# Kernel tuning notes

Hardware: AMD Instinct MI355X
Metric: run time of the kernel (lower is better)

Reference implementation:

```python
import jax, jax.numpy as jnp
import numpy as np

H, D = 8, 16  # heads, head_dim (hidden=128)
NEG_SLOPE = 0.2


def _seg_softmax(logits, seg, n):
    # softmax over edges grouped by destination node (leading axis)
    m = jax.ops.segment_max(logits, seg, num_segments=n)
    m = jnp.where(jnp.isfinite(m), m, 0.0)
    e = jnp.exp(logits - m[seg])
    s = jax.ops.segment_sum(e, seg, num_segments=n)
    return e / (s[seg] + 1e-16)


def _edge_type_out(x_src, x_dst, att_s, att_d, src, dst, n_dst):
    # GAT-style node-level attention for one edge type.
    # x_src: [Ns,H,D], x_dst: [Nd,H,D]
    a_s = (x_src * att_s).sum(-1)            # [Ns,H]
    a_d = (x_dst * att_d).sum(-1)            # [Nd,H]
    alpha = a_s[src] + a_d[dst]              # [E,H]
    alpha = jnp.where(alpha >= 0, alpha, NEG_SLOPE * alpha)  # leaky_relu(0.2)
    alpha = _seg_softmax(alpha, dst, n_dst)  # [E,H]
    msg = x_src[src] * alpha[:, :, None]     # [E,H,D]
    out = jax.ops.segment_sum(msg, dst, num_segments=n_dst)  # [Nd,H,D]
    return jax.nn.relu(out.reshape(n_dst, H * D))


def setup_inputs() -> dict:
    key = jax.random.key(0)
    ks = jax.random.split(key, 24)
    Na, Np, Nd = 300000, 150000, 80000
    E = 1000000
    hid = H * D
    inp = {
        "x_adm": jax.random.normal(ks[0], (Na, 128), jnp.float32),
        "x_pat": jax.random.normal(ks[1], (Np, 64), jnp.float32),
        "x_diag": jax.random.normal(ks[2], (Nd, 64), jnp.float32),
        "e_pa_src": jax.random.randint(ks[3], (E,), 0, Np),
        "e_pa_dst": jax.random.randint(ks[4], (E,), 0, Na),
        "e_da_src": jax.random.randint(ks[5], (E,), 0, Nd),
        "e_da_dst": jax.random.randint(ks[6], (E,), 0, Na),
        # per-node-type projections (PyG HANConv proj[node_type])
        "Wa": jax.random.normal(ks[7], (128, hid), jnp.float32) * 0.05,
        "ba": jnp.zeros((hid,), jnp.float32),
        "Wp": jax.random.normal(ks[8], (64, hid), jnp.float32) * 0.05,
        "bp": jnp.zeros((hid,), jnp.float32),
        "Wd": jax.random.normal(ks[9], (64, hid), jnp.float32) * 0.05,
        "bd": jnp.zeros((hid,), jnp.float32),
        # per-edge-type attention vectors [H,D]
        "ats_pa": jax.random.normal(ks[10], (H, D), jnp.float32) * 0.1,
        "atd_pa": jax.random.normal(ks[11], (H, D), jnp.float32) * 0.1,
        "ats_da": jax.random.normal(ks[12], (H, D), jnp.float32) * 0.1,
        "atd_da": jax.random.normal(ks[13], (H, D), jnp.float32) * 0.1,
        # semantic attention
        "Wk": jax.random.normal(ks[14], (hid, hid), jnp.float32) * 0.05,
        "bk": jnp.zeros((hid,), jnp.float32),
        "q": jax.random.normal(ks[15], (hid,), jnp.float32) * 0.1,
        # final classifier Linear(128, 2)
        "Wl": jax.random.normal(ks[16], (hid, 2), jnp.float32) * 0.05,
        "bl": jnp.zeros((2,), jnp.float32),
    }
    return inp


def reference(x_adm, x_pat, x_diag, e_pa_src, e_pa_dst, e_da_src, e_da_dst,
              Wa, ba, Wp, bp, Wd, bd,
              ats_pa, atd_pa, ats_da, atd_da,
              Wk, bk, q, Wl, bl):
    Na = x_adm.shape[0]
    h_a = (x_adm @ Wa + ba).reshape(Na, H, D)
    h_p = (x_pat @ Wp + bp).reshape(-1, H, D)
    h_d = (x_diag @ Wd + bd).reshape(-1, H, D)
    # node-level attention per metapath (dropout=0.6 skipped: eval mode)
    o_pa = _edge_type_out(h_p, h_a, ats_pa, atd_pa, e_pa_src, e_pa_dst, Na)
    o_da = _edge_type_out(h_d, h_a, ats_da, atd_da, e_da_src, e_da_dst, Na)
    # semantic-level attention across metapaths
    stack = jnp.stack([o_pa, o_da])                 # [2,Na,128]
    w = jnp.tanh(stack @ Wk + bk).mean(axis=1)      # [2,128]
    beta = jax.nn.softmax((w * q).sum(-1), axis=0)  # [2]
    sem = (beta[:, None, None] * stack).sum(0)      # [Na,128]
    logits = sem @ Wl + bl
    return jax.nn.softmax(logits, axis=1)
```

## Files before the change

### kernel.cpp

```cpp
#include <hip/hip_runtime.h>
#include <hip/hip_bf16.h>

typedef __hip_bfloat16 bf16;
typedef __attribute__((ext_vector_type(8))) short frag_ab;
typedef __attribute__((ext_vector_type(4))) float frag_cd;

__device__ __forceinline__ short f2bs(float f){
    bf16 h = __float2bfloat16(f); short s; __builtin_memcpy(&s, &h, 2); return s;
}
__device__ __forceinline__ unsigned pack2(float a, float b){
    return (unsigned)(unsigned short)f2bs(a) | (((unsigned)(unsigned short)f2bs(b)) << 16);
}
__device__ __forceinline__ float blo(unsigned u){ return __uint_as_float(u << 16); }
__device__ __forceinline__ float bhi(unsigned u){ return __uint_as_float(u & 0xffff0000u); }
__device__ __forceinline__ float fast_tanh(float x){
    x = fminf(fmaxf(x, -15.f), 15.f);
    const float t = __expf(2.f*x);
    return (t - 1.f) * __builtin_amdgcn_rcpf(t + 1.f);
}
static inline int imin(int a, int b){ return a < b ? a : b; }

__global__ void prep_fold(const float* __restrict__ Wa, const float* __restrict__ ba,
                          const float* __restrict__ atd_pa, const float* __restrict__ atd_da,
                          float* __restrict__ Wf, float* __restrict__ bdot)
{
    const int k = threadIdx.x;
    for (int g = 0; g < 16; g++){
        const float* att = (g < 8) ? atd_pa : atd_da;
        const int h = g & 7;
        float ssum = 0.f;
        for (int d = 0; d < 16; d++)
            ssum += Wa[k*128 + h*16 + d] * att[h*16 + d];
        Wf[k*16 + g] = ssum;
    }
    if (k < 16){
        const float* att = (k < 8) ? atd_pa : atd_da;
        const int h = k & 7;
        float sb = 0.f;
        for (int d = 0; d < 16; d++) sb += ba[h*16 + d] * att[h*16 + d];
        bdot[k] = sb;
    }
}

__global__ __launch_bounds__(256) void afold_kernel(
    const float* __restrict__ x,
    const float* __restrict__ Wf,
    const float* __restrict__ bdot,
    float* __restrict__ a_pa,
    float* __restrict__ a_da,
    int Na, int ntiles)
{
    __shared__ float WfT[16*132];
    __shared__ float xsr[16*132];
    __shared__ float bs[16];
    const int tid = threadIdx.x;
    for (int i = tid; i < 2048; i += 256){
        const int k = i >> 4, g = i & 15;
        WfT[g*132 + k] = Wf[k*16 + g];
    }
    if (tid < 16) bs[tid] = bdot[tid];
    const int r = tid >> 4, g = tid & 15;

    for (int tile = blockIdx.x; tile < ntiles; tile += gridDim.x){
        const int row0 = tile*16;
        __syncthreads();
        for (int i = tid; i < 512; i += 256){
            const int rr = i >> 5, c4 = (i & 31)*4;
            const int row = row0 + rr;
            float4 v = make_float4(0.f,0.f,0.f,0.f);
            if (row < Na) v = *(const float4*)&x[(size_t)row*128 + c4];
            *(float4*)&xsr[rr*132 + c4] = v;
        }
        __syncthreads();
        float acc = bs[g];
        #pragma unroll 4
        for (int k0 = 0; k0 < 128; k0 += 4){
            const float4 xv = *(const float4*)&xsr[r*132 + k0];
            const float4 wv = *(const float4*)&WfT[g*132 + k0];
            acc += xv.x*wv.x + xv.y*wv.y + xv.z*wv.z + xv.w*wv.w;
        }
        const int row = row0 + r;
        if (row < Na){
            if (g < 8) a_pa[(size_t)row*8 + g]     = acc;
            else       a_da[(size_t)row*8 + (g-8)] = acc;
        }
    }
}

__global__ __launch_bounds__(256) void proj64(
    const float* __restrict__ x,
    const float* __restrict__ W,
    const float* __restrict__ b,
    const float* __restrict__ att0,
    bf16*  __restrict__ h_out,
    float* __restrict__ a0_out,
    int N, int ntiles)
{
    constexpr int K = 64;
    __shared__ float Wsf[K*128];
    __shared__ float xs[32*K];
    const int tid = threadIdx.x;
    const int cg = tid & 31;
    const int rg = tid >> 5;

    for (int i = tid; i < K*32; i += 256)
        *(float4*)&Wsf[i*4] = *(const float4*)&W[i*4];

    float bc[4], at0v[4];
    #pragma unroll
    for (int u = 0; u < 4; u++){ bc[u] = b[cg*4+u]; at0v[u] = att0[cg*4+u]; }
    const int head = cg >> 2;

    for (int tile = blockIdx.x; tile < ntiles; tile += gridDim.x){
        const int row0 = tile*32;
        __syncthreads();
        for (int i = tid; i < 32*(K/4); i += 256){
            const int r  = i / (K/4);
            const int c4 = (i % (K/4))*4;
            const int row = row0 + r;
            float4 v = make_float4(0.f,0.f,0.f,0.f);
            if (row < N) v = *(const float4*)&x[(size_t)row*K + c4];
            *(float4*)&xs[r*K + c4] = v;
        }
        __syncthreads();

        float acc[4][4];
        #pragma unroll
        for (int j = 0; j < 4; j++){ acc[j][0]=acc[j][1]=acc[j][2]=acc[j][3]=0.f; }

        #pragma unroll 2
        for (int k0 = 0; k0 < K; k0 += 4){
            float xr[4][4];
            #pragma unroll
            for (int j = 0; j < 4; j++){
                const float4 v = *(const float4*)&xs[(rg*4+j)*K + k0];
                xr[j][0]=v.x; xr[j][1]=v.y; xr[j][2]=v.z; xr[j][3]=v.w;
            }
            #pragma unroll
            for (int kk = 0; kk < 4; kk++){
                const float4 wv = *(const float4*)&Wsf[(k0+kk)*128 + cg*4];
                #pragma unroll
                for (int j = 0; j < 4; j++){
                    acc[j][0] = fmaf(xr[j][kk], wv.x, acc[j][0]);
                    acc[j][1] = fmaf(xr[j][kk], wv.y, acc[j][1]);
                    acc[j][2] = fmaf(xr[j][kk], wv.z, acc[j][2]);
                    acc[j][3] = fmaf(xr[j][kk], wv.w, acc[j][3]);
                }
            }
        }

        #pragma unroll
        for (int j = 0; j < 4; j++){
            const int row = row0 + rg*4 + j;
            const bool valid = row < N;
            const float h0 = acc[j][0]+bc[0], h1 = acc[j][1]+bc[1];
            const float h2 = acc[j][2]+bc[2], h3 = acc[j][3]+bc[3];
            if (valid){
                h_out[(size_t)row*128 + cg*4+0] = __float2bfloat16(h0);
                h_out[(size_t)row*128 + cg*4+1] = __float2bfloat16(h1);
                h_out[(size_t)row*128 + cg*4+2] = __float2bfloat16(h2);
                h_out[(size_t)row*128 + cg*4+3] = __float2bfloat16(h3);
            }
            float p0 = h0*at0v[0] + h1*at0v[1] + h2*at0v[2] + h3*at0v[3];
            p0 += __shfl_down(p0, 2, 4);
            p0 += __shfl_down(p0, 1, 4);
            if (valid && (cg & 3) == 0) a0_out[(size_t)row*8 + head] = p0;
        }
    }
}

__global__ __launch_bounds__(256) void hist_kernel(
    const int* __restrict__ dst, int* __restrict__ cnt, int E)
{
    const int e = blockIdx.x*256 + threadIdx.x;
    if (e < E) atomicAdd(&cnt[dst[e]], 1);
}

__global__ __launch_bounds__(256) void scan_bsum(
    const int* __restrict__ cnt, int* __restrict__ bsum, int n)
{
    __shared__ int red[256];
    const int base = blockIdx.x*4096;
    int s = 0;
    for (int i = threadIdx.x; i < 4096; i += 256){
        const int idx = base + i;
        s += (idx < n) ? cnt[idx] : 0;
    }
    red[threadIdx.x] = s; __syncthreads();
    for (int st = 128; st > 0; st >>= 1){
        if (threadIdx.x < st) red[threadIdx.x] += red[threadIdx.x + st];
        __syncthreads();
    }
    if (threadIdx.x == 0) bsum[blockIdx.x] = red[0];
}

__global__ __launch_bounds__(256) void scan_excl(int* __restrict__ bsum, int nb)
{
    __shared__ int sh[256];
    const int t = threadIdx.x;
    sh[t] = (t < nb) ? bsum[t] : 0;
    __syncthreads();
    #pragma unroll
    for (int st = 1; st < 256; st <<= 1){
        const int u = (t >= st) ? sh[t - st] : 0;
        __syncthreads();
        sh[t] += u;
        __syncthreads();
    }
    if (t < nb) bsum[t] = t ? sh[t-1] : 0;
}

__global__ __launch_bounds__(256) void scan_write(
    int* __restrict__ cnt,
    const int* __restrict__ bsum,
    int* __restrict__ rowptr, int n)
{
    __shared__ int sh[256];
    const int t = threadIdx.x;
    const int base = blockIdx.x*4096 + t*16;
    int loc[16]; int s = 0;
    #pragma unroll
    for (int i = 0; i < 16; i += 4){
        int4 v = make_int4(0,0,0,0);
        if (base + i + 3 < n) v = *(const int4*)&cnt[base + i];
        else {
            if (base+i   < n) v.x = cnt[base+i];
            if (base+i+1 < n) v.y = cnt[base+i+1];
            if (base+i+2 < n) v.z = cnt[base+i+2];
            if (base+i+3 < n) v.w = cnt[base+i+3];
        }
        loc[i]   = s; s += v.x;
        loc[i+1] = s; s += v.y;
        loc[i+2] = s; s += v.z;
        loc[i+3] = s; s += v.w;
    }
    sh[t] = s; __syncthreads();
    #pragma unroll
    for (int st = 1; st < 256; st <<= 1){
        const int u = (t >= st) ? sh[t - st] : 0;
        __syncthreads();
        sh[t] += u;
        __syncthreads();
    }
    const int off = bsum[blockIdx.x] + (t ? sh[t-1] : 0);
    #pragma unroll
    for (int i = 0; i < 16; i++){
        const int idx = base + i;
        if (idx < n){
            const int v = off + loc[i];
            rowptr[idx] = v;
            cnt[idx]    = v;
        }
    }
    if (blockIdx.x == gridDim.x-1 && t == 255) rowptr[n] = off + s;
}

__global__ __launch_bounds__(256) void scatter_kernel(
    const int* __restrict__ src, const int* __restrict__ dst,
    int* __restrict__ cursor, int* __restrict__ sorted_src, int E)
{
    const int e = blockIdx.x*256 + threadIdx.x;
    if (e < E){
        const int pos = atomicAdd(&cursor[dst[e]], 1);
        sorted_src[pos] = src[e];
    }
}

#define GATHER_EDGE(Ax, Hx) { \
    float lg = (Ax) + ad; \
    lg = lg >= 0.f ? lg : 0.2f*lg; \
    lg = fminf(fmaxf(lg, -30.f), 30.f); \
    const float ee = __expf(lg); \
    acc0 = fmaf(ee, blo(Hx), acc0); \
    acc1 = fmaf(ee, bhi(Hx), acc1); \
    ssum += ee; }

__global__ __launch_bounds__(256) void gather_kernel(
    const int* __restrict__ rowptr, const int* __restrict__ sorted_src,
    const float* __restrict__ a_s,
    const float* __restrict__ a_d,
    const bf16*  __restrict__ h_src,
    unsigned* __restrict__ n_out,
    int Na)
{
    const int n = blockIdx.x*4 + (threadIdx.x >> 6);
    if (n >= Na) return;
    const int l = threadIdx.x & 63;
    const int h = l >> 3;
    const int beg = rowptr[n], end = rowptr[n+1];
    const float ad = a_d[(size_t)n*8 + h];
    const char* hb = (const char*)h_src;
    float acc0 = 0.f, acc1 = 0.f, ssum = 0.f;

    for (int base = beg; base < end; base += 64){
        const int nb = min(64, end - base);
        const int sv = sorted_src[min(base + l, end - 1)];
        for (int k = 0; k < nb; k += 4){
            const int r = nb - k;
            const int i0 = __shfl(sv, k);
            const int i1 = __shfl(sv, r > 1 ? k+1 : k);
            const int i2 = __shfl(sv, r > 2 ? k+2 : k);
            const int i3 = __shfl(sv, r > 3 ? k+3 : k);
            const float    A0 = a_s[(size_t)i0*8 + h];
            const unsigned H0 = *(const unsigned*)(hb + (size_t)i0*256 + l*4);
            const float    A1 = a_s[(size_t)i1*8 + h];
            const unsigned H1 = *(const unsigned*)(hb + (size_t)i1*256 + l*4);
            const float    A2 = a_s[(size_t)i2*8 + h];
            const unsigned H2 = *(const unsigned*)(hb + (size_t)i2*256 + l*4);
            const float    A3 = a_s[(size_t)i3*8 + h];
            const unsigned H3 = *(const unsigned*)(hb + (size_t)i3*256 + l*4);
            GATHER_EDGE(A0, H0)
            if (r > 1) GATHER_EDGE(A1, H1)
            if (r > 2) GATHER_EDGE(A2, H2)
            if (r > 3) GATHER_EDGE(A3, H3)
        }
    }
    const float inv = 1.f/(ssum + 1e-16f);
    n_out[(size_t)n*64 + l] = pack2(fmaxf(acc0*inv, 0.f), fmaxf(acc1*inv, 0.f));
}

#define SEMW_LOADA(dst, t) { \
    const int row_  = (t)*64 + w*16 + m16; \
    const size_t rb_ = (size_t)(row_ < Na ? row_ : Na-1)*64 + quad*4; \
    dst##0 = *(const frag_ab*)&nn[rb_]; \
    dst##1 = *(const frag_ab*)&nn[rb_ + 16]; \
    dst##2 = *(const frag_ab*)&nn[rb_ + 32]; \
    dst##3 = *(const frag_ab*)&nn[rb_ + 48]; }

__global__ __launch_bounds__(256) void semw_mfma(
    const unsigned* __restrict__ np, const unsigned* __restrict__ nd,
    const float* __restrict__ Wk, const float* __restrict__ bk,
    float* __restrict__ wsum, int Na, int nt)
{
    __shared__ short Bs[4*8*64*8];
    __shared__ float csum[4][8][16];
    const int tid  = threadIdx.x;
    const int lane = tid & 63;
    const int w    = tid >> 6;
    const int quad = lane >> 4;
    const int m16  = lane & 15;
    const unsigned* __restrict__ nn = blockIdx.y ? nd : np;

    for (int f = tid; f < 4096; f += 256){
        const float4 v = *(const float4*)&Wk[f*4];
        const int k   = f >> 5;
        const int n4  = (f & 31)*4;
        const int k0i = k >> 5, kr = k & 31;
        const int lnb = (kr >> 3) << 4;
        const int j   = kr & 7;
        const float vv[4] = {v.x, v.y, v.z, v.w};
        #pragma unroll
        for (int t = 0; t < 4; t++){
            const int n = n4 + t;
            Bs[((k0i*8 + (n >> 4))*64 + (lnb | (n & 15)))*8 + j] = f2bs(vv[t]);
        }
    }

    float bkc[8];
    #pragma unroll
    for (int n0i = 0; n0i < 8; n0i++) bkc[n0i] = bk[n0i*16 + m16];
    __syncthreads();

    float colsum[8] = {0.f,0.f,0.f,0.f,0.f,0.f,0.f,0.f};

    int tile = blockIdx.x;
    frag_ab a0 = {}, a1 = {}, a2 = {}, a3 = {};
    frag_ab p0 = {}, p1 = {}, p2 = {}, p3 = {};
    if (tile < nt) SEMW_LOADA(a, tile)
    while (tile < nt){
        const int tnext = tile + gridDim.x;
        if (tnext < nt) SEMW_LOADA(p, tnext)

        frag_cd acc[8];
        #pragma unroll
        for (int n0i = 0; n0i < 8; n0i++) acc[n0i] = (frag_cd){0.f,0.f,0.f,0.f};
        #pragma unroll
        for (int n0i = 0; n0i < 8; n0i++){
            acc[n0i] = __builtin_amdgcn_mfma_f32_16x16x32_bf16(a0,
                *(const frag_ab*)&Bs[((0*8 + n0i)*64 + lane)*8], acc[n0i], 0, 0, 0);
            acc[n0i] = __builtin_amdgcn_mfma_f32_16x16x32_bf16(a1,
                *(const frag_ab*)&Bs[((1*8 + n0i)*64 + lane)*8], acc[n0i], 0, 0, 0);
            acc[n0i] = __builtin_amdgcn_mfma_f32_16x16x32_bf16(a2,
                *(const frag_ab*)&Bs[((2*8 + n0i)*64 + lane)*8], acc[n0i], 0, 0, 0);
            acc[n0i] = __builtin_amdgcn_mfma_f32_16x16x32_bf16(a3,
                *(const frag_ab*)&Bs[((3*8 + n0i)*64 + lane)*8], acc[n0i], 0, 0, 0);
        }

        const int row0 = tile*64 + w*16 + quad*4;
        #pragma unroll
        for (int n0i = 0; n0i < 8; n0i++){
            float part = 0.f;
            #pragma unroll
            for (int r = 0; r < 4; r++)
                if (row0 + r < Na) part += fast_tanh(acc[n0i][r] + bkc[n0i]);
            part += __shfl_down(part, 32);
            part += __shfl_down(part, 16);
            if (lane < 16) colsum[n0i] += part;
        }

        if (tnext < nt){ a0 = p0; a1 = p1; a2 = p2; a3 = p3; }
        tile = tnext;
    }

    if (lane < 16){
        #pragma unroll
        for (int n0i = 0; n0i < 8; n0i++) csum[w][n0i][lane] = colsum[n0i];
    }
    __syncthreads();
    if (tid < 128){
        const int n0i = tid >> 4, l16 = tid & 15;
        const float v = csum[0][n0i][l16] + csum[1][n0i][l16]
                      + csum[2][n0i][l16] + csum[3][n0i][l16];
        unsafeAtomicAdd(&wsum[blockIdx.y*128 + n0i*16 + l16], v);
    }
}

__global__ void beta_kernel(const float* __restrict__ wsum, const float* __restrict__ q,
                            float* __restrict__ beta, float invN)
{
    __shared__ float r0s[128], r1s[128];
    const int tid = threadIdx.x;
    const float qv = q[tid];
    r0s[tid] = wsum[tid]     * invN * qv;
    r1s[tid] = wsum[128+tid] * invN * qv;
    __syncthreads();
    for (int st = 64; st > 0; st >>= 1){
        if (tid < st){ r0s[tid] += r0s[tid+st]; r1s[tid] += r1s[tid+st]; }
        __syncthreads();
    }
    if (tid == 0){
        const float w0 = r0s[0], w1 = r1s[0];
        const float m = fmaxf(w0, w1);
        const float e0 = __expf(w0-m), e1 = __expf(w1-m);
        const float inv = 1.f/(e0+e1);
        beta[0] = e0*inv; beta[1] = e1*inv;
    }
}

__global__ __launch_bounds__(256) void final_kernel(
    const unsigned* __restrict__ n_pa, const unsigned* __restrict__ n_da,
    const float* __restrict__ beta,
    const float* __restrict__ Wl, const float* __restrict__ bl,
    float* __restrict__ out, int Na)
{
    const int gtid = blockIdx.x*256 + threadIdx.x;
    const int node = gtid >> 6;
    const int lane = threadIdx.x & 63;
    if (node >= Na) return;
    const float b0 = beta[0], b1 = beta[1];
    const unsigned up = n_pa[(size_t)node*64 + lane];
    const unsigned ud = n_da[(size_t)node*64 + lane];
    const float sm0 = b0*blo(up) + b1*blo(ud);
    const float sm1 = b0*bhi(up) + b1*bhi(ud);
    const float4 wv = *(const float4*)&Wl[lane*4];
    float l0 = sm0*wv.x + sm1*wv.z;
    float l1 = sm0*wv.y + sm1*wv.w;
    #pragma unroll
    for (int off = 32; off > 0; off >>= 1){
        l0 += __shfl_down(l0, off);
        l1 += __shfl_down(l1, off);
    }
    if (lane == 0){
        l0 += bl[0]; l1 += bl[1];
        const float m = fmaxf(l0, l1);
        const float e0 = __expf(l0-m), e1 = __expf(l1-m);
        const float inv = 1.f/(e0+e1);
        out[(size_t)node*2+0] = e0*inv;
        out[(size_t)node*2+1] = e1*inv;
    }
}

extern "C" void kernel_launch(void* const* d_in, const int* in_sizes, int n_in,
                              void* d_out, int out_size, void* d_ws, size_t ws_size,
                              hipStream_t stream)
{
    const float* x_adm    = (const float*)d_in[0];
    const float* x_pat    = (const float*)d_in[1];
    const float* x_diag   = (const float*)d_in[2];
    const int*   e_pa_src = (const int*)d_in[3];
    const int*   e_pa_dst = (const int*)d_in[4];
    const int*   e_da_src = (const int*)d_in[5];
    const int*   e_da_dst = (const int*)d_in[6];
    const float* Wa = (const float*)d_in[7];
    const float* ba = (const float*)d_in[8];
    const float* Wp = (const float*)d_in[9];
    const float* bp = (const float*)d_in[10];
    const float* Wd = (const float*)d_in[11];
    const float* bd = (const float*)d_in[12];
    const float* ats_pa = (const float*)d_in[13];
    const float* atd_pa = (const float*)d_in[14];
    const float* ats_da = (const float*)d_in[15];
    const float* atd_da = (const float*)d_in[16];
    const float* Wk = (const float*)d_in[17];
    const float* bk = (const float*)d_in[18];
    const float* q  = (const float*)d_in[19];
    const float* Wl = (const float*)d_in[20];
    const float* bl = (const float*)d_in[21];

    const int Na  = in_sizes[0] / 128;
    const int Np  = in_sizes[1] / 64;
    const int Nd  = in_sizes[2] / 64;
    const int Epa = in_sizes[3];
    const int Eda = in_sizes[5];

    float* ws = (float*)d_ws;
    size_t off = 0;
    int*   cnt_pa = (int*)(ws + off); off += Na;
    int*   cnt_da = (int*)(ws + off); off += Na;
    float* wsum   = ws + off; off += 256;
    float* beta   = ws + off; off += 8;
    const size_t zero_len = off;
    off = (off + 3) & ~(size_t)3;
    unsigned* n_pa = (unsigned*)(ws + off); off += (size_t)Na*64;
    unsigned* n_da = (unsigned*)(ws + off); off += (size_t)Na*64;
    float* a_s_pa = ws + off; off += (size_t)Np*8;
    float* a_s_da = ws + off; off += (size_t)Nd*8;
    float* a_d_pa = ws + off; off += (size_t)Na*8;
    float* a_d_da = ws + off; off += (size_t)Na*8;
    float* Wf     = ws + off; off += 2048;
    float* bdot   = ws + off; off += 16;
    bf16*  h_p    = (bf16*)(ws + off); off += (size_t)Np*64;
    bf16*  h_d    = (bf16*)(ws + off); off += (size_t)Nd*64;
    int*   rowptr_pa = (int*)(ws + off); off += (size_t)Na + 1;
    int*   rowptr_da = (int*)(ws + off); off += (size_t)Na + 1;
    int*   sorted_pa = (int*)(ws + off); off += (size_t)Epa;
    int*   sorted_da = (int*)(ws + off); off += (size_t)Eda;
    int*   bsum_pa   = (int*)(ws + off); off += 256;
    int*   bsum_da   = (int*)(ws + off); off += 256;
    (void)n_in; (void)out_size; (void)ws_size; (void)off;

    hipMemsetAsync(d_ws, 0, zero_len*sizeof(float), stream);

    prep_fold<<<1,128,0,stream>>>(Wa, ba, atd_pa, atd_da, Wf, bdot);
    {
        const int nt = (Na + 15)/16;
        afold_kernel<<<imin(nt,4096),256,0,stream>>>(x_adm, Wf, bdot,
                                                     a_d_pa, a_d_da, Na, nt);
    }
    {
        const int nt = (Np + 31)/32;
        proj64<<<imin(nt,1024),256,0,stream>>>(x_pat, Wp, bp, ats_pa, h_p, a_s_pa, Np, nt);
    }
    {
        const int nt = (Nd + 31)/32;
        proj64<<<imin(nt,1024),256,0,stream>>>(x_diag, Wd, bd, ats_da, h_d, a_s_da, Nd, nt);
    }

    const int nbkt = (Na + 4095)/4096;
    hist_kernel<<<(Epa+255)/256, 256, 0, stream>>>(e_pa_dst, cnt_pa, Epa);
    hist_kernel<<<(Eda+255)/256, 256, 0, stream>>>(e_da_dst, cnt_da, Eda);
    scan_bsum<<<nbkt, 256, 0, stream>>>(cnt_pa, bsum_pa, Na);
    scan_bsum<<<nbkt, 256, 0, stream>>>(cnt_da, bsum_da, Na);
    scan_excl<<<1, 256, 0, stream>>>(bsum_pa, nbkt);
    scan_excl<<<1, 256, 0, stream>>>(bsum_da, nbkt);
    scan_write<<<nbkt, 256, 0, stream>>>(cnt_pa, bsum_pa, rowptr_pa, Na);
    scan_write<<<nbkt, 256, 0, stream>>>(cnt_da, bsum_da, rowptr_da, Na);
    scatter_kernel<<<(Epa+255)/256, 256, 0, stream>>>(e_pa_src, e_pa_dst, cnt_pa, sorted_pa, Epa);
    scatter_kernel<<<(Eda+255)/256, 256, 0, stream>>>(e_da_src, e_da_dst, cnt_da, sorted_da, Eda);

    gather_kernel<<<(Na+3)/4, 256, 0, stream>>>(rowptr_pa, sorted_pa,
                                                a_s_pa, a_d_pa, h_p, n_pa, Na);
    gather_kernel<<<(Na+3)/4, 256, 0, stream>>>(rowptr_da, sorted_da,
                                                a_s_da, a_d_da, h_d, n_da, Na);

    {
        const int nt = (Na + 63)/64;
        dim3 grid(imin(nt, 512), 2);
        semw_mfma<<<grid, 256, 0, stream>>>(n_pa, n_da, Wk, bk, wsum, Na, nt);
    }
    beta_kernel<<<1,128,0,stream>>>(wsum, q, beta, 1.f/(float)Na);

    final_kernel<<<(Na+3)/4, 256, 0, stream>>>(n_pa, n_da, beta,
                                               Wl, bl, (float*)d_out, Na);
}
```

Baseline: 936.6 us.

## Use 16-lane groups per node with 128-bit loads and merge both edge-type gathers

The gather kernel now gives each destination node a 16-lane group instead of a full 64-lane wavefront, with each lane loading 16 bytes (8 bf16 values) and keeping eight accumulators. Both edge types are handled in one launch by indexing nodes over 2*Na. The aim is to cut idle lanes for low-degree nodes (around 3.3 edges on average), issue fewer and wider memory requests, and remove one kernel launch. In exchange each lane does more register work and more serial iterations per edge.

```diff
diff --git a/kernel.cpp b/kernel.cpp
--- a/kernel.cpp
+++ b/kernel.cpp
@@ -266,57 +266,64 @@
     }
 }
 
-#define GATHER_EDGE(Ax, Hx) { \
+#define GEDGE(Ax, Hx) { \
     float lg = (Ax) + ad; \
     lg = lg >= 0.f ? lg : 0.2f*lg; \
     lg = fminf(fmaxf(lg, -30.f), 30.f); \
     const float ee = __expf(lg); \
-    acc0 = fmaf(ee, blo(Hx), acc0); \
-    acc1 = fmaf(ee, bhi(Hx), acc1); \
+    acc0 = fmaf(ee, blo(Hx.x), acc0); acc1 = fmaf(ee, bhi(Hx.x), acc1); \
+    acc2 = fmaf(ee, blo(Hx.y), acc2); acc3 = fmaf(ee, bhi(Hx.y), acc3); \
+    acc4 = fmaf(ee, blo(Hx.z), acc4); acc5 = fmaf(ee, bhi(Hx.z), acc5); \
+    acc6 = fmaf(ee, blo(Hx.w), acc6); acc7 = fmaf(ee, bhi(Hx.w), acc7); \
     ssum += ee; }
 
 __global__ __launch_bounds__(256) void gather_kernel(
-    const int* __restrict__ rowptr, const int* __restrict__ sorted_src,
-    const float* __restrict__ a_s,
-    const float* __restrict__ a_d,
-    const bf16*  __restrict__ h_src,
-    unsigned* __restrict__ n_out,
+    const int* __restrict__ rowptr0, const int* __restrict__ sorted0,
+    const float* __restrict__ as0, const float* __restrict__ ad0,
+    const bf16* __restrict__ h0, unsigned* __restrict__ nout0,
+    const int* __restrict__ rowptr1, const int* __restrict__ sorted1,
+    const float* __restrict__ as1, const float* __restrict__ ad1,
+    const bf16* __restrict__ h1, unsigned* __restrict__ nout1,
     int Na)
 {
-    const int n = blockIdx.x*4 + (threadIdx.x >> 6);
-    if (n >= Na) return;
-    const int l = threadIdx.x & 63;
-    const int h = l >> 3;
+    const int gid = blockIdx.x*16 + (threadIdx.x >> 4);
+    const int l   = threadIdx.x & 15;
+    if (gid >= 2*Na) return;
+    const bool ty = gid >= Na;
+    const int n = ty ? gid - Na : gid;
+    const int*   rowptr = ty ? rowptr1 : rowptr0;
+    const int*   sorted = ty ? sorted1 : sorted0;
+    const float* a_s    = ty ? as1 : as0;
+    const char*  hb     = (const char*)(ty ? h1 : h0);
+    unsigned*    nout   = ty ? nout1 : nout0;
+    const int hh  = l >> 1;
+    const float ad = (ty ? ad1 : ad0)[(size_t)n*8 + hh];
+
     const int beg = rowptr[n], end = rowptr[n+1];
-    const float ad = a_d[(size_t)n*8 + h];
-    const char* hb = (const char*)h_src;
-    float acc0 = 0.f, acc1 = 0.f, ssum = 0.f;
-
-    for (int base = beg; base < end; base += 64){
-        const int nb = min(64, end - base);
-        const int sv = sorted_src[min(base + l, end - 1)];
-        for (int k = 0; k < nb; k += 4){
-            const int r = nb - k;
-            const int i0 = __shfl(sv, k);
-            const int i1 = __shfl(sv, r > 1 ? k+1 : k);
-            const int i2 = __shfl(sv, r > 2 ? k+2 : k);
-            const int i3 = __shfl(sv, r > 3 ? k+3 : k);
-            const float    A0 = a_s[(size_t)i0*8 + h];
-            const unsigned H0 = *(const unsigned*)(hb + (size_t)i0*256 + l*4);
-            const float    A1 = a_s[(size_t)i1*8 + h];
-            const unsigned H1 = *(const unsigned*)(hb + (size_t)i1*256 + l*4);
-            const float    A2 = a_s[(size_t)i2*8 + h];
-            const unsigned H2 = *(const unsigned*)(hb + (size_t)i2*256 + l*4);
-            const float    A3 = a_s[(size_t)i3*8 + h];
-            const unsigned H3 = *(const unsigned*)(hb + (size_t)i3*256 + l*4);
-            GATHER_EDGE(A0, H0)
-            if (r > 1) GATHER_EDGE(A1, H1)
-            if (r > 2) GATHER_EDGE(A2, H2)
-            if (r > 3) GATHER_EDGE(A3, H3)
+    float acc0=0.f,acc1=0.f,acc2=0.f,acc3=0.f,acc4=0.f,acc5=0.f,acc6=0.f,acc7=0.f;
+    float ssum=0.f;
+
+    for (int base = beg; base < end; base += 16){
+        const int nb = min(16, end - base);
+        const int sv = sorted[min(base + l, end - 1)];
+        for (int k = 0; k < nb; k += 2){
+            const int i0 = __shfl(sv, k, 16);
+            const int i1 = __shfl(sv, (k+1 < nb) ? k+1 : k, 16);
+            const float A0 = a_s[(size_t)i0*8 + hh];
+            const uint4 H0 = *(const uint4*)(hb + (size_t)i0*256 + l*16);
+            const float A1 = a_s[(size_t)i1*8 + hh];
+            const uint4 H1 = *(const uint4*)(hb + (size_t)i1*256 + l*16);
+            GEDGE(A0, H0)
+            if (k+1 < nb) GEDGE(A1, H1)
         }
     }
     const float inv = 1.f/(ssum + 1e-16f);
-    n_out[(size_t)n*64 + l] = pack2(fmaxf(acc0*inv, 0.f), fmaxf(acc1*inv, 0.f));
+    uint4 u;
+    u.x = pack2(fmaxf(acc0*inv,0.f), fmaxf(acc1*inv,0.f));
+    u.y = pack2(fmaxf(acc2*inv,0.f), fmaxf(acc3*inv,0.f));
+    u.z = pack2(fmaxf(acc4*inv,0.f), fmaxf(acc5*inv,0.f));
+    u.w = pack2(fmaxf(acc6*inv,0.f), fmaxf(acc7*inv,0.f));
+    *(uint4*)&nout[(size_t)n*64 + l*4] = u;
 }
 
 #define SEMW_LOADA(dst, t) { \
@@ -558,10 +565,9 @@
     scatter_kernel<<<(Epa+255)/256, 256, 0, stream>>>(e_pa_src, e_pa_dst, cnt_pa, sorted_pa, Epa);
     scatter_kernel<<<(Eda+255)/256, 256, 0, stream>>>(e_da_src, e_da_dst, cnt_da, sorted_da, Eda);
 
-    gather_kernel<<<(Na+3)/4, 256, 0, stream>>>(rowptr_pa, sorted_pa,
-                                                a_s_pa, a_d_pa, h_p, n_pa, Na);
-    gather_kernel<<<(Na+3)/4, 256, 0, stream>>>(rowptr_da, sorted_da,
-                                                a_s_da, a_d_da, h_d, n_da, Na);
+    gather_kernel<<<(2*Na+15)/16, 256, 0, stream>>>(
+        rowptr_pa, sorted_pa, a_s_pa, a_d_pa, h_p, n_pa,
+        rowptr_da, sorted_da, a_s_da, a_d_da, h_d, n_da, Na);
 
     {
         const int nt = (Na + 63)/64;
```

Result: faster. 877.3 us (-6.3%).
